# Performance work log

Measured on AMD Instinct MI355X. Metric: run time of the kernel, lower is better.

The kernel has to match this reference:

```python
import jax, jax.numpy as jnp
import numpy as np

N_WIN = 7    # n_win hardcoded in AR_Attention
TOPK = 4     # topk routing windows
HEADS = 8    # num_heads


def setup_inputs() -> dict:
    key = jax.random.key(0)
    ks = jax.random.split(key, 6)
    B, H, W, C = 4, 56, 56, 256
    s = 0.02
    x = jax.random.normal(ks[0], (B, H, W, C), jnp.float32)
    Wqkv = jax.random.normal(ks[1], (C, 3 * C), jnp.float32) * s  # Linear(dim, 3*dim) (qk_dim=dim)
    bqkv = jnp.zeros((3 * C,), jnp.float32)
    Wo = jax.random.normal(ks[2], (C, C), jnp.float32) * s        # output projection Linear(dim, dim)
    bo = jnp.zeros((C,), jnp.float32)
    lepe_w = jax.random.normal(ks[3], (5, 5, 1, C), jnp.float32) * s  # 5x5 depthwise conv (side_dwconv=5)
    lepe_b = jnp.zeros((C,), jnp.float32)
    return {"x": x, "Wqkv": Wqkv, "bqkv": bqkv, "Wo": Wo, "bo": bo,
            "lepe_w": lepe_w, "lepe_b": lepe_b}


def reference(x, Wqkv, bqkv, Wo, bo, lepe_w, lepe_b):
    B, H, W, C = x.shape
    nw = N_WIN
    h, w = H // nw, W // nw           # region size (8x8)
    p2 = nw * nw                      # number of regions (49)
    hd = C // HEADS                   # head dim
    scale = float(C) ** -0.5          # qk_scale = qk_dim ** -0.5 (qk_dim = dim)

    # region partition: [B,H,W,C] -> [B,p2,h,w,C]
    xr = x.reshape(B, nw, h, nw, w, C).transpose(0, 1, 3, 2, 4, 5).reshape(B, p2, h, w, C)

    qkv = xr @ Wqkv + bqkv            # [B,p2,h,w,3C]
    q, kv = qkv[..., :C], qkv[..., C:]

    q_pix = q.reshape(B, p2, h * w, C)
    kv_pix = kv.reshape(B, p2, h * w, 2 * C)   # kv_downsample_mode='identity'

    # region-level queries/keys via per-window mean pooling
    q_win = q.mean((2, 3))                     # [B,p2,C]
    k_win = kv[..., :C].mean((2, 3))           # [B,p2,C]

    # LEPE: 5x5 depthwise conv on v over the full image grid
    v_img = kv[..., C:].reshape(B, nw, nw, h, w, C).transpose(0, 1, 3, 2, 4, 5).reshape(B, H, W, C)
    lepe = jax.lax.conv_general_dilated(
        v_img, lepe_w, (1, 1), 'SAME',
        dimension_numbers=('NHWC', 'HWIO', 'NHWC'),
        feature_group_count=C) + lepe_b

    # top-k window routing (param_routing=False, hard routing, mul_weight='none')
    r_logit = jnp.einsum('bpc,bqc->bpq', q_win * scale, k_win)  # [B,p2,p2]
    _, r_idx = jax.lax.top_k(r_logit, TOPK)                     # [B,p2,TOPK]

    # gather selected kv windows: [B,p2,TOPK,h*w,2C]
    kv_sel = jax.vmap(lambda kvp, i: kvp[i])(kv_pix, r_idx)

    k_sel = kv_sel[..., :C].reshape(B, p2, TOPK * h * w, HEADS, hd)
    v_sel = kv_sel[..., C:].reshape(B, p2, TOPK * h * w, HEADS, hd)
    qh = q_pix.reshape(B, p2, h * w, HEADS, hd)

    attn = jnp.einsum('bpqnd,bpknd->bpnqk', qh * scale, k_sel)  # [B,p2,heads,hw,TOPK*hw]
    attn = jax.nn.softmax(attn, axis=-1)
    out = jnp.einsum('bpnqk,bpknd->bpqnd', attn, v_sel).reshape(B, p2, h, w, C)

    # windows back to image grid
    out = out.reshape(B, nw, nw, h, w, C).transpose(0, 1, 3, 2, 4, 5).reshape(B, H, W, C)
    out = out + lepe
    return out @ Wo + bo
```

## Files before the change

kernel.cpp:

```cpp
#include <hip/hip_runtime.h>
#include <hip/hip_bf16.h>

#define NPIX 12544

typedef short bf16x8 __attribute__((ext_vector_type(8)));
typedef short bf16x4 __attribute__((ext_vector_type(4)));
typedef float f32x4  __attribute__((ext_vector_type(4)));

__device__ __forceinline__ float bf2f(unsigned short u) {
    unsigned int x = ((unsigned int)u) << 16;
    float f; __builtin_memcpy(&f, &x, sizeof(f)); return f;
}
__device__ __forceinline__ unsigned short f2bf(float f) {
    __hip_bfloat16 h = __float2bfloat16(f);
    unsigned short u; __builtin_memcpy(&u, &h, 2); return u;
}
__device__ __forceinline__ void load_lds16(const unsigned short* g, unsigned short* l) {
    __builtin_amdgcn_global_load_lds(
        (const __attribute__((address_space(1))) unsigned int*)g,
        (__attribute__((address_space(3))) unsigned int*)l,
        16, 0, 0);
}
__device__ __forceinline__ unsigned ldsoff(const void* p) {
    return (unsigned)(unsigned long long)(const __attribute__((address_space(3))) char*)p;
}
template<int OFF>
__device__ __forceinline__ bf16x4 tr16(unsigned addr) {
    bf16x4 d;
    asm volatile("ds_read_b64_tr_b16 %0, %1 offset:%c2"
                 : "=v"(d) : "v"(addr), "i"(OFF));
    return d;
}

__global__ __launch_bounds__(256) void k_prep(
    const float* __restrict__ X, unsigned short* __restrict__ Xb,
    float* __restrict__ xmean,
    const float* __restrict__ Wqkv, const float* __restrict__ Wo,
    unsigned short* __restrict__ Wtq, unsigned short* __restrict__ Wto)
{
    __shared__ __align__(16) unsigned char sm[64 * 65 * 4];
    const int t = threadIdx.x;
    const int blk = blockIdx.x;
    if (blk < 392) {
        float* part = (float*)sm;
        const int w = blk >> 1, hc = blk & 1;
        const int b = w / 49, p = w % 49;
        const int wi = p / 7, wj = p % 7;
        const int ch0 = hc * 128;
        const int ps = t >> 5, cg = t & 31;
        float4 s = {0.f, 0.f, 0.f, 0.f};
        #pragma unroll
        for (int i = 0; i < 8; i++) {
            int pp = ps * 8 + i;
            int y = wi * 8 + (pp >> 3), x = wj * 8 + (pp & 7);
            int idx = (((b * 56) + y) * 56 + x) * 256 + ch0 + cg * 4;
            float4 v = *reinterpret_cast<const float4*>(X + idx);
            s.x += v.x; s.y += v.y; s.z += v.z; s.w += v.w;
            ushort4 o = { f2bf(v.x), f2bf(v.y), f2bf(v.z), f2bf(v.w) };
            *reinterpret_cast<ushort4*>(Xb + idx) = o;
        }
        *reinterpret_cast<float4*>(part + t * 4) = *reinterpret_cast<float4*>(&s);
        __syncthreads();
        if (t < 32) {
            float4 m = {0.f, 0.f, 0.f, 0.f};
            #pragma unroll
            for (int ps2 = 0; ps2 < 8; ps2++) {
                float4 v = *reinterpret_cast<float4*>(part + (ps2 * 32 + t) * 4);
                m.x += v.x; m.y += v.y; m.z += v.z; m.w += v.w;
            }
            m.x *= (1.f / 64.f); m.y *= (1.f / 64.f);
            m.z *= (1.f / 64.f); m.w *= (1.f / 64.f);
            *reinterpret_cast<float4*>(xmean + w * 256 + ch0 + t * 4) = m;
        }
    } else {
        float* tile = (float*)sm;
        int tb = blk - 392;
        const float* Wsrc; unsigned short* Wdst; int N, kt, nt;
        if (tb < 48) { Wsrc = Wqkv; Wdst = Wtq; N = 768; kt = tb / 12; nt = tb % 12; }
        else { tb -= 48; Wsrc = Wo; Wdst = Wto; N = 256; kt = tb / 4; nt = tb % 4; }
        const int k0 = kt * 64, n0 = nt * 64;
        const int r0 = t >> 6, c = t & 63;
        #pragma unroll
        for (int i = 0; i < 16; i++) {
            int r = i * 4 + r0;
            tile[r * 65 + c] = Wsrc[(size_t)(k0 + r) * N + n0 + c];
        }
        __syncthreads();
        #pragma unroll
        for (int i = 0; i < 16; i++) {
            int n = i * 4 + r0;
            Wdst[(size_t)(n0 + n) * 256 + k0 + c] = f2bf(tile[c * 65 + n]);
        }
    }
}

__global__ __launch_bounds__(256) void k_main1(
    const unsigned short* __restrict__ A,
    const unsigned short* __restrict__ Bt,
    const float* __restrict__ bias,
    unsigned short* __restrict__ O,
    const float* __restrict__ xmean,
    const float* __restrict__ Wqkv,
    float* __restrict__ qwin, float* __restrict__ kwin)
{
    __shared__ __align__(16) unsigned char sm1[32768];
    const int t = threadIdx.x;
    const int blk = blockIdx.x;
    if (blk < 588) {
        unsigned short* As = (unsigned short*)sm1;
        unsigned short* Bs = (unsigned short*)(sm1 + 16384);
        const int m0 = (blk % 98) * 128, n0 = (blk / 98) * 128;
        const int wave = t >> 6, lane = t & 63, quad = lane >> 4, lo = lane & 15;
        const int wm = wave & 1, wn = wave >> 1;
        const int sr = wave * 16 + (lane >> 2);
        const int sc = lane & 3;
        f32x4 acc[4][4];
        #pragma unroll
        for (int i = 0; i < 4; i++)
            #pragma unroll
            for (int j = 0; j < 4; j++) acc[i][j] = (f32x4){0.f, 0.f, 0.f, 0.f};

        auto stage = [&](int it) {
            int kt = it * 32;
            unsigned short* Ad = As + (it & 1) * 4096;
            unsigned short* Bd = Bs + (it & 1) * 4096;
            #pragma unroll
            for (int j = 0; j < 2; j++) {
                int row = j * 64 + sr;
                int e = sc ^ ((row >> 1) & 3);
                load_lds16(A  + (size_t)(m0 + row) * 256 + kt + e * 8, &Ad[row * 32 + sc * 8]);
                load_lds16(Bt + (size_t)(n0 + row) * 256 + kt + e * 8, &Bd[row * 32 + sc * 8]);
            }
        };
        stage(0);
        for (int it = 0; it < 8; ++it) {
            if (it < 7) {
                stage(it + 1);
                asm volatile("s_waitcnt vmcnt(4)" ::: "memory");
            } else {
                asm volatile("s_waitcnt vmcnt(0)" ::: "memory");
            }
            __builtin_amdgcn_s_barrier();
            const unsigned short* Ac = As + (it & 1) * 4096;
            const unsigned short* Bc = Bs + (it & 1) * 4096;
            bf16x8 af[4], bfr[4];
            #pragma unroll
            for (int mt = 0; mt < 4; mt++) {
                int row = wm * 64 + mt * 16 + lo;
                int c = quad ^ ((row >> 1) & 3);
                af[mt] = *reinterpret_cast<const bf16x8*>(&Ac[row * 32 + c * 8]);
            }
            #pragma unroll
            for (int nt = 0; nt < 4; nt++) {
                int col = wn * 64 + nt * 16 + lo;
                int c = quad ^ ((col >> 1) & 3);
                bfr[nt] = *reinterpret_cast<const bf16x8*>(&Bc[col * 32 + c * 8]);
            }
            #pragma unroll
            for (int mt = 0; mt < 4; mt++)
                #pragma unroll
                for (int nt = 0; nt < 4; nt++)
                    acc[mt][nt] = __builtin_amdgcn_mfma_f32_16x16x32_bf16(
                        af[mt], bfr[nt], acc[mt][nt], 0, 0, 0);
            __builtin_amdgcn_s_barrier();
        }
        float bv[4];
        #pragma unroll
        for (int nt = 0; nt < 4; nt++) bv[nt] = bias[n0 + wn * 64 + nt * 16 + lo];
        #pragma unroll
        for (int mt = 0; mt < 4; mt++)
            #pragma unroll
            for (int nt = 0; nt < 4; nt++) {
                int n = n0 + wn * 64 + nt * 16 + lo;
                #pragma unroll
                for (int r = 0; r < 4; r++) {
                    int m = m0 + wm * 64 + mt * 16 + quad * 4 + r;
                    O[m * 768 + n] = f2bf(acc[mt][nt][r] + bv[nt]);
                }
            }
    } else {
        float* xs = (float*)sm1;
        const int u = blk - 588;
        const int bp = u % 196;
        const int half = u / 196;
        const int c = t;
        xs[c] = xmean[bp * 256 + c];
        __syncthreads();
        const int col = half * 256 + c;
        float a = 0.f;
        for (int k = 0; k < 256; k++) a += xs[k] * Wqkv[k * 768 + col];
        float* outp = half ? kwin : qwin;
        outp[bp * 256 + c] = a + bias[col];
    }
}

__global__ __launch_bounds__(256) void k_main2(
    const float* __restrict__ qwin, const float* __restrict__ kwin,
    int* __restrict__ ridx)
{
    __shared__ __align__(16) unsigned char sm2[1024];
    const int t = threadIdx.x;
    const int blk = blockIdx.x;
    float* part = (float*)sm2;
    float* lg   = (float*)(sm2 + 49 * 4 * 4);
    const int b = blk / 49, p = blk % 49;
    if (t < 196) {
        int d = t >> 2, pr = t & 3;
        const float* qp = &qwin[(b * 49 + p) * 256];
        const float* kp = &kwin[(b * 49 + d) * 256];
        float a = 0.f;
        for (int ch = pr * 64; ch < pr * 64 + 64; ch++) a += qp[ch] * kp[ch];
        part[d * 4 + pr] = a;
    }
    __syncthreads();
    if (t < 49) lg[t] = part[t * 4 + 0] + part[t * 4 + 1] + part[t * 4 + 2] + part[t * 4 + 3];
    __syncthreads();
    if (t == 0) {
        unsigned long long used = 0ull;
        for (int sel = 0; sel < 4; sel++) {
            float best = -1e30f; int bi = 0;
            for (int qq = 0; qq < 49; qq++)
                if (!((used >> qq) & 1ull) && lg[qq] > best) { best = lg[qq]; bi = qq; }
            used |= (1ull << bi);
            ridx[blk * 4 + sel] = bi;
        }
    }
}

__global__ __launch_bounds__(256) void k_attn(
    const unsigned short* __restrict__ QKV,
    const int* __restrict__ ridx,
    const float* __restrict__ lw, const float* __restrict__ lb,
    unsigned short* __restrict__ Osum)
{
    __shared__ __align__(16) unsigned char smem[52352];
    unsigned short* Vs  = (unsigned short*)smem;
    unsigned short* Qs  = (unsigned short*)(smem + 16384);
    unsigned short* Ks  = (unsigned short*)(smem + 21504);
    unsigned short* PST = (unsigned short*)(smem + 16384);
    float* lws          = (float*)(smem + 49152);

    const int p = blockIdx.x, head = blockIdx.y, b = blockIdx.z;
    const int t = threadIdx.x;
    const int wi = p / 7, wj = p % 7;
    const int wave = t >> 6, lane = t & 63, quad = lane >> 4, lo = lane & 15;
    const int pix4 = t >> 2, c4 = t & 3;

    if (t < 200) {
        int tap = t >> 3, ci = (t & 7) * 4;
        *reinterpret_cast<float4*>(&lws[tap * 32 + ci]) =
            *reinterpret_cast<const float4*>(lw + tap * 256 + head * 32 + ci);
    }
    {
        int y = wi * 8 + (pix4 >> 3), x = wj * 8 + (pix4 & 7);
        const unsigned short* qp = QKV + (((b * 56) + y) * 56 + x) * 768 + head * 32 + c4 * 8;
        bf16x8 v = *reinterpret_cast<const bf16x8*>(qp);
        int sw = c4 ^ ((pix4 >> 3) & 3);
        *reinterpret_cast<bf16x8*>(&Qs[pix4 * 40 + sw * 8]) = v;
    }
    #pragma unroll
    for (int pass = 0; pass < 4; pass++) {
        int sel = ridx[(b * 49 + p) * 4 + pass];
        int si = sel / 7, sj = sel % 7;
        int y = si * 8 + (pix4 >> 3), x = sj * 8 + (pix4 & 7);
        const unsigned short* base = QKV + (((b * 56) + y) * 56 + x) * 768 + 256 + head * 32;
        bf16x8 kv = *reinterpret_cast<const bf16x8*>(base + c4 * 8);
        bf16x8 vv = *reinterpret_cast<const bf16x8*>(base + 256 + c4 * 8);
        int krow = pass * 64 + pix4;
        int sw = c4 ^ ((krow >> 3) & 3);
        *reinterpret_cast<bf16x8*>(&Ks[krow * 40 + sw * 8]) = kv;
        *reinterpret_cast<bf16x8*>(
            &Vs[(krow >> 2) * 128 + (c4 >> 1) * 64 + (krow & 3) * 16 + (c4 & 1) * 8]) = vv;
    }
    __syncthreads();

    float lep[8];
    {
        int q = wave * 16 + lo;
        int py = wi * 8 + (q >> 3), px = wj * 8 + (q & 7);
        float4 b0 = *reinterpret_cast<const float4*>(lb + head * 32 + quad * 8);
        float4 b1 = *reinterpret_cast<const float4*>(lb + head * 32 + quad * 8 + 4);
        lep[0] = b0.x; lep[1] = b0.y; lep[2] = b0.z; lep[3] = b0.w;
        lep[4] = b1.x; lep[5] = b1.y; lep[6] = b1.z; lep[7] = b1.w;
        #pragma unroll
        for (int ky = 0; ky < 5; ky++) {
            int yy = py + ky - 2;
            if (yy < 0 || yy >= 56) continue;
            #pragma unroll
            for (int kx = 0; kx < 5; kx++) {
                int xx = px + kx - 2;
                if (xx < 0 || xx >= 56) continue;
                bf16x8 v = *reinterpret_cast<const bf16x8*>(
                    QKV + (((b * 56) + yy) * 56 + xx) * 768 + 512 + head * 32 + quad * 8);
                const float* wrow = &lws[(ky * 5 + kx) * 32 + quad * 8];
                float4 w0 = *reinterpret_cast<const float4*>(wrow);
                float4 w1 = *reinterpret_cast<const float4*>(wrow + 4);
                lep[0] += bf2f((unsigned short)v[0]) * w0.x;
                lep[1] += bf2f((unsigned short)v[1]) * w0.y;
                lep[2] += bf2f((unsigned short)v[2]) * w0.z;
                lep[3] += bf2f((unsigned short)v[3]) * w0.w;
                lep[4] += bf2f((unsigned short)v[4]) * w1.x;
                lep[5] += bf2f((unsigned short)v[5]) * w1.y;
                lep[6] += bf2f((unsigned short)v[6]) * w1.z;
                lep[7] += bf2f((unsigned short)v[7]) * w1.w;
            }
        }
    }

    f32x4 sc[16];
    {
        int row = wave * 16 + lo;
        bf16x8 af = *reinterpret_cast<const bf16x8*>(
            &Qs[row * 40 + ((quad ^ ((row >> 3) & 3)) * 8)]);
        f32x4 z = (f32x4){0.f, 0.f, 0.f, 0.f};
        #pragma unroll
        for (int nt = 0; nt < 16; nt++) {
            int key = nt * 16 + lo;
            bf16x8 bfr = *reinterpret_cast<const bf16x8*>(
                &Ks[key * 40 + ((quad ^ ((key >> 3) & 3)) * 8)]);
            sc[nt] = __builtin_amdgcn_mfma_f32_16x16x32_bf16(af, bfr, z, 0, 0, 0);
        }
    }
    float M[4] = {-1e30f, -1e30f, -1e30f, -1e30f};
    #pragma unroll
    for (int nt = 0; nt < 16; nt++)
        #pragma unroll
        for (int r = 0; r < 4; r++) M[r] = fmaxf(M[r], sc[nt][r] * 0.0625f);
    #pragma unroll
    for (int d = 1; d < 16; d <<= 1)
        #pragma unroll
        for (int r = 0; r < 4; r++) M[r] = fmaxf(M[r], __shfl_xor(M[r], d));
    float l[4] = {0.f, 0.f, 0.f, 0.f};
    #pragma unroll
    for (int nt = 0; nt < 16; nt++)
        #pragma unroll
        for (int r = 0; r < 4; r++) {
            float e = __expf(sc[nt][r] * 0.0625f - M[r]);
            sc[nt][r] = e;
            l[r] += e;
        }
    #pragma unroll
    for (int d = 1; d < 16; d <<= 1)
        #pragma unroll
        for (int r = 0; r < 4; r++) l[r] += __shfl_xor(l[r], d);

    __syncthreads();

    unsigned short* myP = PST + wave * 4096;
    #pragma unroll
    for (int nt = 0; nt < 16; nt++) {
        ushort4 pk = { f2bf(sc[nt][0]), f2bf(sc[nt][1]),
                       f2bf(sc[nt][2]), f2bf(sc[nt][3]) };
        *reinterpret_cast<ushort4*>(&myP[(nt * 16 + lo) * 16 + quad * 4]) = pk;
    }
    const unsigned paddr = ldsoff(myP) + quad * 256 + lo * 8;
    const unsigned vaddr = ldsoff(Vs)  + quad * 512 + lo * 8;
    asm volatile("s_waitcnt lgkmcnt(0)" ::: "memory");
    __builtin_amdgcn_sched_barrier(0);

    bf16x4 ra0, ra1, rw00, rw01, rw10, rw11;
    ra0  = tr16<0>(paddr);
    ra1  = tr16<128>(paddr);
    rw00 = tr16<0>(vaddr);
    rw01 = tr16<256>(vaddr);
    rw10 = tr16<128>(vaddr);
    rw11 = tr16<384>(vaddr);
    f32x4 o0 = (f32x4){0.f, 0.f, 0.f, 0.f}, o1 = o0;
    #pragma unroll
    for (int kt = 0; kt < 8; kt++) {
        bf16x4 na0, na1, nw00, nw01, nw10, nw11;
        if (kt < 7) {
            unsigned pn = paddr + (kt + 1) * 1024;
            unsigned vn = vaddr + (kt + 1) * 2048;
            na0  = tr16<0>(pn);
            na1  = tr16<128>(pn);
            nw00 = tr16<0>(vn);
            nw01 = tr16<256>(vn);
            nw10 = tr16<128>(vn);
            nw11 = tr16<384>(vn);
            asm volatile("s_waitcnt lgkmcnt(6)" ::: "memory");
        } else {
            asm volatile("s_waitcnt lgkmcnt(0)" ::: "memory");
        }
        __builtin_amdgcn_sched_barrier(0);
        bf16x8 pa, vb0, vb1;
        #pragma unroll
        for (int j = 0; j < 4; j++) {
            pa[j]  = ra0[j];  pa[4 + j]  = ra1[j];
            vb0[j] = rw00[j]; vb0[4 + j] = rw01[j];
            vb1[j] = rw10[j]; vb1[4 + j] = rw11[j];
        }
        o0 = __builtin_amdgcn_mfma_f32_16x16x32_bf16(pa, vb0, o0, 0, 0, 0);
        o1 = __builtin_amdgcn_mfma_f32_16x16x32_bf16(pa, vb1, o1, 0, 0, 0);
        if (kt < 7) { ra0 = na0; ra1 = na1; rw00 = nw00; rw01 = nw01; rw10 = nw10; rw11 = nw11; }
    }

    {
        unsigned short* ow = myP;
        float i0 = 1.f / l[0], i1 = 1.f / l[1], i2 = 1.f / l[2], i3 = 1.f / l[3];
        ushort4 p0 = { f2bf(o0[0] * i0), f2bf(o0[1] * i1),
                       f2bf(o0[2] * i2), f2bf(o0[3] * i3) };
        ushort4 p1 = { f2bf(o1[0] * i0), f2bf(o1[1] * i1),
                       f2bf(o1[2] * i2), f2bf(o1[3] * i3) };
        *reinterpret_cast<ushort4*>(&ow[lo * 16 + quad * 4]) = p0;
        *reinterpret_cast<ushort4*>(&ow[(16 + lo) * 16 + quad * 4]) = p1;
    }
    const unsigned oaddr = ldsoff(PST) + wave * 8192 + quad * 256 + lo * 8;
    asm volatile("s_waitcnt lgkmcnt(0)" ::: "memory");
    __builtin_amdgcn_sched_barrier(0);
    bf16x4 e0 = tr16<0>(oaddr);
    bf16x4 e1 = tr16<128>(oaddr);
    asm volatile("s_waitcnt lgkmcnt(0)" ::: "memory");
    __builtin_amdgcn_sched_barrier(0);
    {
        int q = wave * 16 + lo;
        int y = wi * 8 + (q >> 3), x = wj * 8 + (q & 7);
        size_t gbase = (size_t)(((b * 56) + y) * 56 + x) * 256 + head * 32 + quad * 8;
        bf16x8 oo;
        #pragma unroll
        for (int j = 0; j < 4; j++) {
            oo[j]     = (short)f2bf(bf2f((unsigned short)e0[j]) + lep[j]);
            oo[4 + j] = (short)f2bf(bf2f((unsigned short)e1[j]) + lep[4 + j]);
        }
        *reinterpret_cast<bf16x8*>(Osum + gbase) = oo;
    }
}

__global__ __launch_bounds__(256) void k_proj(
    const unsigned short* __restrict__ A,
    const unsigned short* __restrict__ Bt,
    const float* __restrict__ bias,
    float* __restrict__ O)
{
    __shared__ __align__(16) unsigned short As[2 * 128 * 32];
    __shared__ __align__(16) unsigned short Bs[2 * 64 * 32];
    const int t = threadIdx.x;
    const int m0 = blockIdx.x * 128, n0 = blockIdx.y * 64;
    const int wave = t >> 6, lane = t & 63, quad = lane >> 4, lo = lane & 15;
    const int sr = wave * 16 + (lane >> 2);
    const int sc = lane & 3;
    f32x4 acc[2][4];
    #pragma unroll
    for (int i = 0; i < 2; i++)
        #pragma unroll
        for (int j = 0; j < 4; j++) acc[i][j] = (f32x4){0.f, 0.f, 0.f, 0.f};

    auto stage = [&](int it) {
        int kt = it * 32;
        unsigned short* Ad = As + (it & 1) * 4096;
        unsigned short* Bd = Bs + (it & 1) * 2048;
        #pragma unroll
        for (int j = 0; j < 2; j++) {
            int row = j * 64 + sr;
            int e = sc ^ ((row >> 1) & 3);
            load_lds16(A + (size_t)(m0 + row) * 256 + kt + e * 8, &Ad[row * 32 + sc * 8]);
        }
        {
            int e = sc ^ ((sr >> 1) & 3);
            load_lds16(Bt + (size_t)(n0 + sr) * 256 + kt + e * 8, &Bd[sr * 32 + sc * 8]);
        }
    };
    stage(0);
    for (int it = 0; it < 8; ++it) {
        if (it < 7) {
            stage(it + 1);
            asm volatile("s_waitcnt vmcnt(3)" ::: "memory");
        } else {
            asm volatile("s_waitcnt vmcnt(0)" ::: "memory");
        }
        __builtin_amdgcn_s_barrier();
        const unsigned short* Ac = As + (it & 1) * 4096;
        const unsigned short* Bc = Bs + (it & 1) * 2048;
        bf16x8 af[2], bfr[4];
        #pragma unroll
        for (int mt = 0; mt < 2; mt++) {
            int row = wave * 32 + mt * 16 + lo;
            int c = quad ^ ((row >> 1) & 3);
            af[mt] = *reinterpret_cast<const bf16x8*>(&Ac[row * 32 + c * 8]);
        }
        #pragma unroll
        for (int nt = 0; nt < 4; nt++) {
            int col = nt * 16 + lo;
            int c = quad ^ ((col >> 1) & 3);
            bfr[nt] = *reinterpret_cast<const bf16x8*>(&Bc[col * 32 + c * 8]);
        }
        #pragma unroll
        for (int mt = 0; mt < 2; mt++)
            #pragma unroll
            for (int nt = 0; nt < 4; nt++)
                acc[mt][nt] = __builtin_amdgcn_mfma_f32_16x16x32_bf16(
                    af[mt], bfr[nt], acc[mt][nt], 0, 0, 0);
        __builtin_amdgcn_s_barrier();
    }
    float bv[4];
    #pragma unroll
    for (int nt = 0; nt < 4; nt++) bv[nt] = bias[n0 + nt * 16 + lo];
    #pragma unroll
    for (int mt = 0; mt < 2; mt++)
        #pragma unroll
        for (int nt = 0; nt < 4; nt++) {
            int n = n0 + nt * 16 + lo;
            #pragma unroll
            for (int r = 0; r < 4; r++) {
                int m = m0 + wave * 32 + mt * 16 + quad * 4 + r;
                O[m * 256 + n] = acc[mt][nt][r] + bv[nt];
            }
        }
}

extern "C" void kernel_launch(void* const* d_in, const int* in_sizes, int n_in,
                              void* d_out, int out_size, void* d_ws, size_t ws_size,
                              hipStream_t stream)
{
    const float* x    = (const float*)d_in[0];
    const float* Wqkv = (const float*)d_in[1];
    const float* bqkv = (const float*)d_in[2];
    const float* Wo   = (const float*)d_in[3];
    const float* bo   = (const float*)d_in[4];
    const float* lw   = (const float*)d_in[5];
    const float* lb   = (const float*)d_in[6];
    float* out = (float*)d_out;

    char* ws = (char*)d_ws;
    size_t off = 0;
    unsigned short* qkv   = (unsigned short*)(ws + off); off += (size_t)NPIX * 768 * 2;
    unsigned short* xb    = (unsigned short*)(ws + off); off += (size_t)NPIX * 256 * 2;
    unsigned short* Wtq   = (unsigned short*)(ws + off); off += 768 * 256 * 2;
    unsigned short* Wto   = (unsigned short*)(ws + off); off += 256 * 256 * 2;
    unsigned short* Osum  = (unsigned short*)(ws + off); off += (size_t)NPIX * 256 * 2;
    float* xmean = (float*)(ws + off); off += 196 * 256 * 4;
    float* qwin  = (float*)(ws + off); off += 196 * 256 * 4;
    float* kwin  = (float*)(ws + off); off += 196 * 256 * 4;
    int*   ridx  = (int*)(ws + off);   off += 196 * 4 * 4;

    k_prep <<<dim3(456),      256, 0, stream>>>(x, xb, xmean, Wqkv, Wo, Wtq, Wto);
    k_main1<<<dim3(980),      256, 0, stream>>>(xb, Wtq, bqkv, qkv, xmean, Wqkv, qwin, kwin);
    k_main2<<<dim3(196),      256, 0, stream>>>(qwin, kwin, ridx);
    k_attn <<<dim3(49, 8, 4), 256, 0, stream>>>(qkv, ridx, lw, lb, Osum);
    k_proj <<<dim3(98, 4),    256, 0, stream>>>(Osum, Wto, bo, out);
}
```

Before: 164.7 us.

## Shrink attention kernel LDS footprint and raise occupancy to four blocks per CU

The attention kernel now loads Q fragments straight from global memory into registers, so the Q staging area in LDS goes away. The P·V product is split into two halves, which lets each wave's P staging buffer shrink by half, and shared memory drops from about 52KB to 40KB. Launch bounds now request four blocks per CU. The LEPE conv loop clamps its addresses and masks out-of-range taps instead of branching, and the routing indices come in as one int4 load. In exchange there is an extra waitcnt between the halves, possible register pressure under the new bound, and redundant loads at the image borders.

```diff
diff --git a/kernel.cpp b/kernel.cpp
--- a/kernel.cpp
+++ b/kernel.cpp
@@ -227,18 +227,17 @@
     }
 }
 
-__global__ __launch_bounds__(256) void k_attn(
+__global__ __launch_bounds__(256, 4) void k_attn(
     const unsigned short* __restrict__ QKV,
     const int* __restrict__ ridx,
     const float* __restrict__ lw, const float* __restrict__ lb,
     unsigned short* __restrict__ Osum)
 {
-    __shared__ __align__(16) unsigned char smem[52352];
+    __shared__ __align__(16) unsigned char smem[40064];
     unsigned short* Vs  = (unsigned short*)smem;
-    unsigned short* Qs  = (unsigned short*)(smem + 16384);
-    unsigned short* Ks  = (unsigned short*)(smem + 21504);
+    unsigned short* Ks  = (unsigned short*)(smem + 16384);
     unsigned short* PST = (unsigned short*)(smem + 16384);
-    float* lws          = (float*)(smem + 49152);
+    float* lws          = (float*)(smem + 36864);
 
     const int p = blockIdx.x, head = blockIdx.y, b = blockIdx.z;
     const int t = threadIdx.x;
@@ -246,72 +245,72 @@
     const int wave = t >> 6, lane = t & 63, quad = lane >> 4, lo = lane & 15;
     const int pix4 = t >> 2, c4 = t & 3;
 
+    const int q  = wave * 16 + lo;
+    const int qy = wi * 8 + (q >> 3), qx = wj * 8 + (q & 7);
+
+    bf16x8 af = *reinterpret_cast<const bf16x8*>(
+        QKV + (size_t)(((b * 56) + qy) * 56 + qx) * 768 + head * 32 + quad * 8);
+
     if (t < 200) {
         int tap = t >> 3, ci = (t & 7) * 4;
         *reinterpret_cast<float4*>(&lws[tap * 32 + ci]) =
             *reinterpret_cast<const float4*>(lw + tap * 256 + head * 32 + ci);
     }
     {
-        int y = wi * 8 + (pix4 >> 3), x = wj * 8 + (pix4 & 7);
-        const unsigned short* qp = QKV + (((b * 56) + y) * 56 + x) * 768 + head * 32 + c4 * 8;
-        bf16x8 v = *reinterpret_cast<const bf16x8*>(qp);
-        int sw = c4 ^ ((pix4 >> 3) & 3);
-        *reinterpret_cast<bf16x8*>(&Qs[pix4 * 40 + sw * 8]) = v;
-    }
-    #pragma unroll
-    for (int pass = 0; pass < 4; pass++) {
-        int sel = ridx[(b * 49 + p) * 4 + pass];
-        int si = sel / 7, sj = sel % 7;
-        int y = si * 8 + (pix4 >> 3), x = sj * 8 + (pix4 & 7);
-        const unsigned short* base = QKV + (((b * 56) + y) * 56 + x) * 768 + 256 + head * 32;
-        bf16x8 kv = *reinterpret_cast<const bf16x8*>(base + c4 * 8);
-        bf16x8 vv = *reinterpret_cast<const bf16x8*>(base + 256 + c4 * 8);
-        int krow = pass * 64 + pix4;
-        int sw = c4 ^ ((krow >> 3) & 3);
-        *reinterpret_cast<bf16x8*>(&Ks[krow * 40 + sw * 8]) = kv;
-        *reinterpret_cast<bf16x8*>(
-            &Vs[(krow >> 2) * 128 + (c4 >> 1) * 64 + (krow & 3) * 16 + (c4 & 1) * 8]) = vv;
+        const int4 rs = *reinterpret_cast<const int4*>(&ridx[(b * 49 + p) * 4]);
+        const int sels[4] = { rs.x, rs.y, rs.z, rs.w };
+        #pragma unroll
+        for (int pass = 0; pass < 4; pass++) {
+            int sel = sels[pass];
+            int si = sel / 7, sj = sel % 7;
+            int y = si * 8 + (pix4 >> 3), x = sj * 8 + (pix4 & 7);
+            const unsigned short* base = QKV + (((b * 56) + y) * 56 + x) * 768 + 256 + head * 32;
+            bf16x8 kv = *reinterpret_cast<const bf16x8*>(base + c4 * 8);
+            bf16x8 vv = *reinterpret_cast<const bf16x8*>(base + 256 + c4 * 8);
+            int krow = pass * 64 + pix4;
+            int sw = c4 ^ ((krow >> 3) & 3);
+            *reinterpret_cast<bf16x8*>(&Ks[krow * 40 + sw * 8]) = kv;
+            *reinterpret_cast<bf16x8*>(
+                &Vs[(krow >> 2) * 128 + (c4 >> 1) * 64 + (krow & 3) * 16 + (c4 & 1) * 8]) = vv;
+        }
     }
     __syncthreads();
 
     float lep[8];
     {
-        int q = wave * 16 + lo;
-        int py = wi * 8 + (q >> 3), px = wj * 8 + (q & 7);
         float4 b0 = *reinterpret_cast<const float4*>(lb + head * 32 + quad * 8);
         float4 b1 = *reinterpret_cast<const float4*>(lb + head * 32 + quad * 8 + 4);
         lep[0] = b0.x; lep[1] = b0.y; lep[2] = b0.z; lep[3] = b0.w;
         lep[4] = b1.x; lep[5] = b1.y; lep[6] = b1.z; lep[7] = b1.w;
         #pragma unroll
         for (int ky = 0; ky < 5; ky++) {
-            int yy = py + ky - 2;
-            if (yy < 0 || yy >= 56) continue;
+            int yy = qy + ky - 2;
+            int yc = min(max(yy, 0), 55);
+            bool yin = (yy >= 0) & (yy < 56);
             #pragma unroll
             for (int kx = 0; kx < 5; kx++) {
-                int xx = px + kx - 2;
-                if (xx < 0 || xx >= 56) continue;
+                int xx = qx + kx - 2;
+                int xc = min(max(xx, 0), 55);
+                float mf = (yin & (xx >= 0) & (xx < 56)) ? 1.f : 0.f;
                 bf16x8 v = *reinterpret_cast<const bf16x8*>(
-                    QKV + (((b * 56) + yy) * 56 + xx) * 768 + 512 + head * 32 + quad * 8);
+                    QKV + (size_t)(((b * 56) + yc) * 56 + xc) * 768 + 512 + head * 32 + quad * 8);
                 const float* wrow = &lws[(ky * 5 + kx) * 32 + quad * 8];
                 float4 w0 = *reinterpret_cast<const float4*>(wrow);
                 float4 w1 = *reinterpret_cast<const float4*>(wrow + 4);
-                lep[0] += bf2f((unsigned short)v[0]) * w0.x;
-                lep[1] += bf2f((unsigned short)v[1]) * w0.y;
-                lep[2] += bf2f((unsigned short)v[2]) * w0.z;
-                lep[3] += bf2f((unsigned short)v[3]) * w0.w;
-                lep[4] += bf2f((unsigned short)v[4]) * w1.x;
-                lep[5] += bf2f((unsigned short)v[5]) * w1.y;
-                lep[6] += bf2f((unsigned short)v[6]) * w1.z;
-                lep[7] += bf2f((unsigned short)v[7]) * w1.w;
+                lep[0] += bf2f((unsigned short)v[0]) * w0.x * mf;
+                lep[1] += bf2f((unsigned short)v[1]) * w0.y * mf;
+                lep[2] += bf2f((unsigned short)v[2]) * w0.z * mf;
+                lep[3] += bf2f((unsigned short)v[3]) * w0.w * mf;
+                lep[4] += bf2f((unsigned short)v[4]) * w1.x * mf;
+                lep[5] += bf2f((unsigned short)v[5]) * w1.y * mf;
+                lep[6] += bf2f((unsigned short)v[6]) * w1.z * mf;
+                lep[7] += bf2f((unsigned short)v[7]) * w1.w * mf;
             }
         }
     }
 
     f32x4 sc[16];
     {
-        int row = wave * 16 + lo;
-        bf16x8 af = *reinterpret_cast<const bf16x8*>(
-            &Qs[row * 40 + ((quad ^ ((row >> 3) & 3)) * 8)]);
         f32x4 z = (f32x4){0.f, 0.f, 0.f, 0.f};
         #pragma unroll
         for (int nt = 0; nt < 16; nt++) {
@@ -346,66 +345,70 @@
 
     __syncthreads();
 
-    unsigned short* myP = PST + wave * 4096;
-    #pragma unroll
-    for (int nt = 0; nt < 16; nt++) {
-        ushort4 pk = { f2bf(sc[nt][0]), f2bf(sc[nt][1]),
-                       f2bf(sc[nt][2]), f2bf(sc[nt][3]) };
-        *reinterpret_cast<ushort4*>(&myP[(nt * 16 + lo) * 16 + quad * 4]) = pk;
-    }
-    const unsigned paddr = ldsoff(myP) + quad * 256 + lo * 8;
-    const unsigned vaddr = ldsoff(Vs)  + quad * 512 + lo * 8;
-    asm volatile("s_waitcnt lgkmcnt(0)" ::: "memory");
-    __builtin_amdgcn_sched_barrier(0);
-
-    bf16x4 ra0, ra1, rw00, rw01, rw10, rw11;
-    ra0  = tr16<0>(paddr);
-    ra1  = tr16<128>(paddr);
-    rw00 = tr16<0>(vaddr);
-    rw01 = tr16<256>(vaddr);
-    rw10 = tr16<128>(vaddr);
-    rw11 = tr16<384>(vaddr);
+    unsigned short* myP = PST + wave * 2048;
+    const unsigned pbase = ldsoff(myP) + quad * 256 + lo * 8;
+    const unsigned vbase = ldsoff(Vs)  + quad * 512 + lo * 8;
     f32x4 o0 = (f32x4){0.f, 0.f, 0.f, 0.f}, o1 = o0;
     #pragma unroll
-    for (int kt = 0; kt < 8; kt++) {
-        bf16x4 na0, na1, nw00, nw01, nw10, nw11;
-        if (kt < 7) {
-            unsigned pn = paddr + (kt + 1) * 1024;
-            unsigned vn = vaddr + (kt + 1) * 2048;
-            na0  = tr16<0>(pn);
-            na1  = tr16<128>(pn);
-            nw00 = tr16<0>(vn);
-            nw01 = tr16<256>(vn);
-            nw10 = tr16<128>(vn);
-            nw11 = tr16<384>(vn);
-            asm volatile("s_waitcnt lgkmcnt(6)" ::: "memory");
-        } else {
-            asm volatile("s_waitcnt lgkmcnt(0)" ::: "memory");
-        }
+    for (int h = 0; h < 2; h++) {
+        #pragma unroll
+        for (int nt2 = 0; nt2 < 8; nt2++) {
+            int nt = h * 8 + nt2;
+            ushort4 pk = { f2bf(sc[nt][0]), f2bf(sc[nt][1]),
+                           f2bf(sc[nt][2]), f2bf(sc[nt][3]) };
+            *reinterpret_cast<ushort4*>(&myP[(nt2 * 16 + lo) * 16 + quad * 4]) = pk;
+        }
+        asm volatile("s_waitcnt lgkmcnt(0)" ::: "memory");
         __builtin_amdgcn_sched_barrier(0);
-        bf16x8 pa, vb0, vb1;
-        #pragma unroll
-        for (int j = 0; j < 4; j++) {
-            pa[j]  = ra0[j];  pa[4 + j]  = ra1[j];
-            vb0[j] = rw00[j]; vb0[4 + j] = rw01[j];
-            vb1[j] = rw10[j]; vb1[4 + j] = rw11[j];
-        }
-        o0 = __builtin_amdgcn_mfma_f32_16x16x32_bf16(pa, vb0, o0, 0, 0, 0);
-        o1 = __builtin_amdgcn_mfma_f32_16x16x32_bf16(pa, vb1, o1, 0, 0, 0);
-        if (kt < 7) { ra0 = na0; ra1 = na1; rw00 = nw00; rw01 = nw01; rw10 = nw10; rw11 = nw11; }
+
+        const unsigned vb = vbase + h * 8192;
+        bf16x4 ra0, ra1, rw00, rw01, rw10, rw11;
+        ra0  = tr16<0>(pbase);
+        ra1  = tr16<128>(pbase);
+        rw00 = tr16<0>(vb);
+        rw01 = tr16<256>(vb);
+        rw10 = tr16<128>(vb);
+        rw11 = tr16<384>(vb);
+        #pragma unroll
+        for (int kt = 0; kt < 4; kt++) {
+            bf16x4 na0, na1, nw00, nw01, nw10, nw11;
+            if (kt < 3) {
+                unsigned pn = pbase + (kt + 1) * 1024;
+                unsigned vn = vb + (kt + 1) * 2048;
+                na0  = tr16<0>(pn);
+                na1  = tr16<128>(pn);
+                nw00 = tr16<0>(vn);
+                nw01 = tr16<256>(vn);
+                nw10 = tr16<128>(vn);
+                nw11 = tr16<384>(vn);
+                asm volatile("s_waitcnt lgkmcnt(6)" ::: "memory");
+            } else {
+                asm volatile("s_waitcnt lgkmcnt(0)" ::: "memory");
+            }
+            __builtin_amdgcn_sched_barrier(0);
+            bf16x8 pa, vb0, vb1;
+            #pragma unroll
+            for (int j = 0; j < 4; j++) {
+                pa[j]  = ra0[j];  pa[4 + j]  = ra1[j];
+                vb0[j] = rw00[j]; vb0[4 + j] = rw01[j];
+                vb1[j] = rw10[j]; vb1[4 + j] = rw11[j];
+            }
+            o0 = __builtin_amdgcn_mfma_f32_16x16x32_bf16(pa, vb0, o0, 0, 0, 0);
+            o1 = __builtin_amdgcn_mfma_f32_16x16x32_bf16(pa, vb1, o1, 0, 0, 0);
+            if (kt < 3) { ra0 = na0; ra1 = na1; rw00 = nw00; rw01 = nw01; rw10 = nw10; rw11 = nw11; }
+        }
     }
 
     {
-        unsigned short* ow = myP;
         float i0 = 1.f / l[0], i1 = 1.f / l[1], i2 = 1.f / l[2], i3 = 1.f / l[3];
         ushort4 p0 = { f2bf(o0[0] * i0), f2bf(o0[1] * i1),
                        f2bf(o0[2] * i2), f2bf(o0[3] * i3) };
         ushort4 p1 = { f2bf(o1[0] * i0), f2bf(o1[1] * i1),
                        f2bf(o1[2] * i2), f2bf(o1[3] * i3) };
-        *reinterpret_cast<ushort4*>(&ow[lo * 16 + quad * 4]) = p0;
-        *reinterpret_cast<ushort4*>(&ow[(16 + lo) * 16 + quad * 4]) = p1;
-    }
-    const unsigned oaddr = ldsoff(PST) + wave * 8192 + quad * 256 + lo * 8;
+        *reinterpret_cast<ushort4*>(&myP[lo * 16 + quad * 4]) = p0;
+        *reinterpret_cast<ushort4*>(&myP[(16 + lo) * 16 + quad * 4]) = p1;
+    }
+    const unsigned oaddr = ldsoff(myP) + quad * 256 + lo * 8;
     asm volatile("s_waitcnt lgkmcnt(0)" ::: "memory");
     __builtin_amdgcn_sched_barrier(0);
     bf16x4 e0 = tr16<0>(oaddr);
@@ -413,9 +416,7 @@
     asm volatile("s_waitcnt lgkmcnt(0)" ::: "memory");
     __builtin_amdgcn_sched_barrier(0);
     {
-        int q = wave * 16 + lo;
-        int y = wi * 8 + (q >> 3), x = wj * 8 + (q & 7);
-        size_t gbase = (size_t)(((b * 56) + y) * 56 + x) * 256 + head * 32 + quad * 8;
+        size_t gbase = (size_t)(((b * 56) + qy) * 56 + qx) * 256 + head * 32 + quad * 8;
         bf16x8 oo;
         #pragma unroll
         for (int j = 0; j < 4; j++) {
```

Result: slower. 218.9 us (+32.9%).
